# Optimization experiments

Measured on AMD Instinct MI355X. Metric: run time of the kernel, lower is better.

The kernel has to match this reference:

```python
import jax, jax.numpy as jnp
import numpy as np

EPS = 1e-5

def bn(x, p, axis):
    # p: (4,C) = [gamma, beta, running_mean, running_var]; eval-mode batchnorm
    g, b, m, v = p
    shp = [1] * x.ndim
    shp[axis] = -1
    g = g.reshape(shp); b = b.reshape(shp); m = m.reshape(shp); v = v.reshape(shp)
    return (x - m) * g * jax.lax.rsqrt(v + EPS) + b

def knn_idx(query, ref, k):
    # query (B,S,D), ref (B,N,D) -> (B,S,k) nearest-neighbor indices
    d = (jnp.sum(query * query, -1)[:, :, None]
         - 2.0 * jnp.einsum('bsd,bnd->bsn', query, ref)
         + jnp.sum(ref * ref, -1)[:, None, :])
    return jax.lax.top_k(-d, k)[1]

def fps(xyz, npoint):
    # farthest point sampling, deterministic start at index 0. xyz (B,N,3) -> (B,npoint)
    B, N, _ = xyz.shape
    def body(i, state):
        idxs, dists, far = state
        idxs = idxs.at[:, i].set(far)
        centroid = jnp.take_along_axis(xyz, far[:, None, None], axis=1)  # (B,1,3)
        d = jnp.sum((xyz - centroid) ** 2, -1)                           # (B,N)
        dists = jnp.minimum(dists, d)
        return idxs, dists, jnp.argmax(dists, -1).astype(jnp.int32)
    idxs = jnp.zeros((B, npoint), jnp.int32)
    dists = jnp.full((B, N), 1e10, xyz.dtype)
    far = jnp.zeros((B,), jnp.int32)
    idxs, _, _ = jax.lax.fori_loop(0, npoint, body, (idxs, dists, far))
    return idxs

def sample_and_group(npoint, nsample, xyz, feature):
    # xyz (B,N,3); feature (B,C,N) channel-first -> new_xyz (B,S,3), new_feature (B,S,k,2C)
    B = xyz.shape[0]
    xyz_sg = jax.lax.stop_gradient(xyz)
    fps_idx = fps(xyz_sg, npoint)                       # (B,S)
    bi = jnp.arange(B)[:, None]
    new_xyz = xyz[bi, fps_idx]                          # (B,S,3)
    ft = jnp.swapaxes(feature, 1, 2)                    # (B,N,C)
    new_pts = ft[bi, fps_idx]                           # (B,S,C)
    idx = knn_idx(jax.lax.stop_gradient(new_xyz), xyz_sg, nsample)  # (B,S,k)
    grouped = ft[jnp.arange(B)[:, None, None], idx]     # (B,S,k,C)
    centered = grouped - new_pts[:, :, None, :]
    new_feature = jnp.concatenate(
        [centered, jnp.broadcast_to(new_pts[:, :, None, :], grouped.shape)], -1)
    return new_xyz, new_feature

def local_op(x, w, bnp):
    # x (B,S,k,D); conv1d k=1 over D, bn, relu, max over neighbors -> (B,out,S)
    h = jax.nn.relu(bn(jnp.einsum('bskd,od->bsko', x, w), bnp, -1))
    return jnp.swapaxes(jnp.max(h, axis=2), 1, 2)

def edge_branch(f_t, idx, w, bnp):
    # DGCNN-style EdgeConv: concat(f_j - f_i, f_i), conv2d k=1, bn, leakyrelu, max over k
    B = f_t.shape[0]
    nb = f_t[jnp.arange(B)[:, None, None], idx]         # (B,N,k,C)
    center = jnp.broadcast_to(f_t[:, :, None, :], nb.shape)
    e = jnp.concatenate([nb - center, center], -1)      # (B,N,k,2C)
    h = jax.nn.leaky_relu(bn(jnp.einsum('bnkc,oc->bnko', e, w), bnp, -1), 0.2)
    return jnp.max(h, axis=2)                           # (B,N,C)

def dual_graph_fusion(xyz_cf, f, k, geo_w, geo_bn, feat_w, feat_bn, fuse_w, fuse_bn):
    # xyz_cf (B,3,N), f (B,C,N): one kNN graph in coordinate space, one in feature space,
    # EdgeConv on each, concat, 1x1 conv fusion -> (B,C,N)
    xyz_t = jax.lax.stop_gradient(jnp.swapaxes(xyz_cf, 1, 2))  # (B,N,3)
    f_t = jnp.swapaxes(f, 1, 2)                                # (B,N,C)
    idx_g = knn_idx(xyz_t, xyz_t, k)
    f_sg = jax.lax.stop_gradient(f_t)
    idx_f = knn_idx(f_sg, f_sg, k)
    g = edge_branch(f_t, idx_g, geo_w, geo_bn)
    h = edge_branch(f_t, idx_f, feat_w, feat_bn)
    fused = jnp.concatenate([g, h], -1)                        # (B,N,2C)
    out = jax.nn.leaky_relu(bn(jnp.einsum('bnc,oc->bno', fused, fuse_w), fuse_bn, -1), 0.2)
    return jnp.swapaxes(out, 1, 2)                             # (B,C,N)

def _bn_params(key, c):
    k1, k2, k3, k4 = jax.random.split(key, 4)
    g = jax.random.uniform(k1, (c,), minval=0.5, maxval=1.5)
    b = jax.random.normal(k2, (c,)) * 0.1
    m = jax.random.normal(k3, (c,)) * 0.1
    v = jax.random.uniform(k4, (c,), minval=0.5, maxval=1.5)
    return jnp.stack([g, b, m, v])

def setup_inputs() -> dict:
    key = jax.random.key(0)
    ks = jax.random.split(key, 20)
    B, N = 16, 2048
    def w(k, o, i):
        return jax.random.normal(k, (o, i), dtype=jnp.float32) * (1.0 / np.sqrt(i))
    return {
        'x': jax.random.normal(ks[0], (B, 6, N), dtype=jnp.float32),
        'w1': w(ks[1], 64, 6),        'bn1': _bn_params(ks[2], 64),
        'w2': w(ks[3], 1024, 64),     'bn2': _bn_params(ks[4], 1024),
        'geo_w': w(ks[5], 64, 128),   'geo_bn': _bn_params(ks[6], 64),
        'feat_w': w(ks[7], 64, 128),  'feat_bn': _bn_params(ks[8], 64),
        'fuse_w': w(ks[9], 64, 128),  'fuse_bn': _bn_params(ks[10], 64),
        'gl0_w': w(ks[11], 128, 128), 'gl0_bn': _bn_params(ks[12], 128),
        'gl1_w': w(ks[13], 256, 256), 'gl1_bn': _bn_params(ks[14], 256),
        'wf': w(ks[15], 512, 1280),   'bnf': _bn_params(ks[16], 512),
    }

def reference(x, w1, bn1, w2, bn2, geo_w, geo_bn, feat_w, feat_bn, fuse_w, fuse_bn,
              gl0_w, gl0_bn, gl1_w, gl1_bn, wf, bnf):
    B, _, N = x.shape
    xyz = jnp.swapaxes(x[:, 0:3, :], 1, 2)                                   # (B,N,3)
    f_o = jax.nn.relu(bn(jnp.einsum('bcn,oc->bon', x, w1), bn1, 1))          # (B,64,N)
    out_feat = dual_graph_fusion(x[:, 0:3, :], f_o, 20,
                                 geo_w, geo_bn, feat_w, feat_bn, fuse_w, fuse_bn)
    stride = N // 256
    x_skip = jax.nn.relu(bn(jnp.einsum('bcn,oc->bon', f_o[:, :, ::stride], w2), bn2, 1))  # (B,1024,256)
    new_xyz, nf = sample_and_group(512, 32, xyz, out_feat)
    f0 = local_op(nf, gl0_w, gl0_bn)                                         # (B,128,512)
    new_xyz, nf = sample_and_group(256, 32, new_xyz, f0)
    f1 = local_op(nf, gl1_w, gl1_bn)                                         # (B,256,256)
    f1 = jnp.concatenate([f1, x_skip], 1)                                    # (B,1280,256)
    res = jax.nn.leaky_relu(bn(jnp.einsum('bcn,oc->bon', f1, wf), bnf, 1), 0.2)  # (B,512,256)
    return res
```

## Files before the change

kernel.cpp:

```cpp
#include <hip/hip_runtime.h>
#include <float.h>
#include <math.h>


static constexpr int B_   = 16;
static constexpr int N_   = 2048;
static constexpr int NP1  = 512;
static constexpr int NP2  = 256;
static constexpr int KG   = 20;
static constexpr int NSAMP= 32;
static constexpr int CHQ  = 256;

static constexpr long OFF_FT   = 0;
static constexpr long OFF_SQ   = OFF_FT   + (long)B_*N_*64;
static constexpr long OFF_BIG  = OFF_SQ   + (long)B_*N_;
static constexpr long OFF_IDXG = OFF_BIG  + (long)B_*N_*256;
static constexpr long OFF_IDXF = OFF_IDXG + (long)B_*N_*KG;
static constexpr long OFF_OUTF = OFF_IDXF + (long)B_*N_*KG;
static constexpr long OFF_FPS1 = OFF_OUTF + (long)B_*N_*64;
static constexpr long OFF_NX1  = OFF_FPS1 + (long)B_*NP1;
static constexpr long OFF_IDX1 = OFF_NX1  + (long)B_*NP1*3;
static constexpr long OFF_F0T  = OFF_IDX1 + (long)B_*NP1*NSAMP;
static constexpr long OFF_FPS2 = OFF_F0T  + (long)B_*NP1*128;
static constexpr long OFF_NX2  = OFF_FPS2 + (long)B_*NP2;
static constexpr long OFF_IDX2 = OFF_NX2  + (long)B_*NP2*3;
static constexpr long OFF_Q1   = OFF_IDX2 + (long)B_*NP2*NSAMP;
static constexpr long OFF_V    = OFF_Q1   + (long)B_*NP1*512;
static constexpr long OFF_WPP  = OFF_V    + (long)B_*NP2*1280;
static constexpr long OFF_WPQ0 = OFF_WPP  + 256*64;
static constexpr long OFF_WPQ1 = OFF_WPQ0 + 256*64;
static constexpr long OFF_WFT  = OFF_WPQ1 + 512*128;
static constexpr long OFF_SC   = OFF_WFT  + 128*64;
static constexpr long OFF_DL1  = OFF_SC   + 4352;
static constexpr long OFF_DL2  = OFF_DL1  + (long)B_*256*8;
static constexpr long OFF_ST   = OFF_DL2  + (long)B_*512;

static constexpr int SC_S1=0, SC_T1=64, SC_SGEO=128, SC_TGEO=192, SC_SFEAT=256, SC_TFEAT=320,
   SC_SFUSE=384, SC_TFUSE=448, SC_SGL0=512, SC_TGL0=640, SC_SGL1=768, SC_TGL1=1024,
   SC_S2=1280, SC_T2=2304, SC_SF=3328, SC_TF=3840;

__device__ __forceinline__ float lrelu_(float x) { return x >= 0.0f ? x : 0.2f * x; }

template<int CTRL, int RM>
__device__ __forceinline__ float dpp_maxm(float v) {
    int o = __builtin_amdgcn_update_dpp(__float_as_int(v), __float_as_int(v),
                                        CTRL, RM, 0xF, false);
    return fmaxf(v, __int_as_float(o));
}
__device__ __forceinline__ float wave_max64_sgpr(float v) {
    v = dpp_maxm<0xB1, 0xF>(v);
    v = dpp_maxm<0x4E, 0xF>(v);
    v = dpp_maxm<0x141,0xF>(v);
    v = dpp_maxm<0x140,0xF>(v);
    v = dpp_maxm<0x142,0xA>(v);
    v = dpp_maxm<0x143,0xC>(v);
    return __int_as_float(__builtin_amdgcn_readlane(__float_as_int(v), 63));
}

template<int CTRL>
__device__ __forceinline__ unsigned dpp_minu(unsigned x) {
    unsigned o = (unsigned)__builtin_amdgcn_update_dpp(0, (int)x, CTRL, 0xF, 0xF, true);
    return o < x ? o : x;
}
__device__ __forceinline__ unsigned wave_minu(unsigned x) {
    x = dpp_minu<0xB1>(x);
    x = dpp_minu<0x4E>(x);
    x = dpp_minu<0x141>(x);
    x = dpp_minu<0x140>(x);
    { unsigned o = (unsigned)__shfl_xor((int)x, 16); x = o < x ? o : x; }
    { unsigned o = (unsigned)__shfl_xor((int)x, 32); x = o < x ? o : x; }
    return x;
}

__device__ __forceinline__ unsigned sortable_(float f) {
    unsigned u = __float_as_uint(f);
    return u ^ ((unsigned)((int)u >> 31) | 0x80000000u);
}

__global__ void k_prep(const float* __restrict__ bn1, const float* __restrict__ bn2,
                       const float* __restrict__ geow, const float* __restrict__ geobn,
                       const float* __restrict__ featw, const float* __restrict__ featbn,
                       const float* __restrict__ fusew, const float* __restrict__ fusebn,
                       const float* __restrict__ gl0w, const float* __restrict__ gl0bn,
                       const float* __restrict__ gl1w, const float* __restrict__ gl1bn,
                       const float* __restrict__ bnfp, float* __restrict__ ws)
{
    const int tid = blockIdx.x * blockDim.x + threadIdx.x;
    const int nt  = gridDim.x * blockDim.x;
    float* sc = ws + OFF_SC;
    {
        const float* ps[8]  = {bn1, geobn, featbn, fusebn, gl0bn, gl1bn, bn2, bnfp};
        const int    ch[8]  = {64, 64, 64, 64, 128, 256, 1024, 512};
        const int    so[8]  = {SC_S1, SC_SGEO, SC_SFEAT, SC_SFUSE, SC_SGL0, SC_SGL1, SC_S2, SC_SF};
        const int    to[8]  = {SC_T1, SC_TGEO, SC_TFEAT, SC_TFUSE, SC_TGL0, SC_TGL1, SC_T2, SC_TF};
        for (int g = 0; g < 8; g++) {
            const float* p = ps[g]; int C = ch[g];
            for (int i = tid; i < C; i += nt) {
                float gg = p[i], bb = p[C+i], mm = p[2*C+i], vv = p[3*C+i];
                float s = gg * (1.0f / sqrtf(vv + 1e-5f));
                sc[so[g] + i] = s;
                sc[to[g] + i] = bb - mm * s;
            }
        }
    }
    for (int j = tid; j < 256*64; j += nt) {
        int o = j >> 6, c = j & 63; float v;
        if      (o < 64)  v = geow[o*128 + c];
        else if (o < 128) v = geow[(o-64)*128 + 64 + c];
        else if (o < 192) v = featw[(o-128)*128 + c];
        else              v = featw[(o-192)*128 + 64 + c];
        ws[OFF_WPP + j] = v;
    }
    for (int j = tid; j < 256*64; j += nt) {
        int o = j >> 6, c = j & 63; float v;
        if (o < 128) v = gl0w[o*128 + c];
        else         v = gl0w[(o-128)*128 + 64 + c] - gl0w[(o-128)*128 + c];
        ws[OFF_WPQ0 + j] = v;
    }
    for (int j = tid; j < 512*128; j += nt) {
        int o = j >> 7, c = j & 127; float v;
        if (o < 256) v = gl1w[o*256 + c];
        else         v = gl1w[(o-256)*256 + 128 + c] - gl1w[(o-256)*256 + c];
        ws[OFF_WPQ1 + j] = v;
    }
    for (int j = tid; j < 128*64; j += nt) {
        int c = j >> 6, o = j & 63;
        ws[OFF_WFT + j] = fusew[o*128 + c];
    }
}

__global__ void __launch_bounds__(256) k_feat0(const float* __restrict__ x,
                                               const float* __restrict__ w1,
                                               const float* __restrict__ sc,
                                               float* __restrict__ ft, float* __restrict__ sq)
{
    const int t = threadIdx.x, lane = t & 63, w = t >> 6;
    const int pid = blockIdx.x*4 + w;
    const int b = pid >> 11, n = pid & (N_-1);
    const float* xb = x + (long)b*6*N_ + n;
    float acc = 0.0f;
    #pragma unroll
    for (int c = 0; c < 6; c++) acc += w1[lane*6 + c] * xb[(long)c*N_];
    float val = fmaxf(sc[SC_S1 + lane]*acc + sc[SC_T1 + lane], 0.0f);
    ft[((long)b*N_ + n)*64 + lane] = val;
    float v2 = val*val;
    #pragma unroll
    for (int s = 1; s < 64; s <<= 1) v2 += __shfl_xor(v2, s);
    if (lane == 0) sq[b*N_ + n] = v2;
}

template<int RPL, int KSEL>
__device__ __forceinline__ void topk_sel3(float (&v)[RPL], int lane, int* __restrict__ out)
{
    unsigned key[RPL];
    #pragma unroll
    for (int j = 0; j < RPL; j++) key[j] = sortable_(v[j]);

    unsigned consumed = 0;
    unsigned m1 = key[0]; int s1 = 0;
    unsigned m2 = 0xFFFFFFFFu; int s2 = 0;
    #pragma unroll
    for (int j = 1; j < RPL; j++) {
        unsigned kk = key[j];
        bool lt1 = kk < m1;
        bool lt2 = kk < m2;
        unsigned nm2 = lt1 ? m1 : (lt2 ? kk : m2);
        int      ns2 = lt1 ? s1 : (lt2 ? j  : s2);
        m1 = lt1 ? kk : m1;
        s1 = lt1 ? j  : s1;
        m2 = nm2; s2 = ns2;
    }
    #pragma unroll 1
    for (int k = 0; k < KSEL; k++) {
        unsigned g = wave_minu(m1);
        unsigned long long cand = __ballot(m1 == g);
        int gi;
        if (__popcll(cand) > 1) {
            int ci = (m1 == g) ? (s1*64 + lane) : 0x7FFFFFFF;
            #pragma unroll
            for (int s = 1; s < 64; s <<= 1) { int o = __shfl_xor(ci, s); ci = o < ci ? o : ci; }
            gi = ci;
        } else {
            int wl = __ffsll((long long)cand) - 1;
            gi = __builtin_amdgcn_readlane(s1, wl) * 64 + wl;
        }
        if (lane == 0) out[k] = gi;
        if (k + 1 < KSEL) {
            bool win = (m1 == g) && (s1*64 + lane == gi);
            if (win) {
                consumed |= 1u << s1;
                m1 = m2; s1 = s2;
                m2 = 0xFFFFFFFFu;
            }
            bool need = win && (m1 == 0xFFFFFFFFu);
            if (__any(need)) {
                if (need) {
                    m1 = 0xFFFFFFFFu; s1 = 0; m2 = 0xFFFFFFFFu; s2 = 0;
                    #pragma unroll
                    for (int j = 0; j < RPL; j++) {
                        unsigned kk = ((consumed >> j) & 1u) ? 0xFFFFFFFFu : key[j];
                        bool lt1 = kk < m1;
                        bool lt2 = kk < m2;
                        unsigned nm2 = lt1 ? m1 : (lt2 ? kk : m2);
                        int      ns2 = lt1 ? s1 : (lt2 ? j  : s2);
                        m1 = lt1 ? kk : m1;
                        s1 = lt1 ? j  : s1;
                        m2 = nm2; s2 = ns2;
                    }
                }
            }
        }
    }
}

template<int NREF, int RPL, int KSEL>
__device__ __forceinline__ void knn_gbody(
    const float* qp, long qBatch, int qsN, int qsD, int NQ,
    const float* rp, long rBatch, long rsN, long rsD,
    int* out, int bid)
{
    const int t = threadIdx.x, lane = t & 63, w = t >> 6;
    const int bpb = NQ / 4;
    const int b = bid / bpb;
    const int qi = (bid % bpb)*4 + w;
    const float* rb = rp + (long)b*rBatch;
    const float* qb = qp + (long)b*qBatch + (long)qi*qsN;
    float qx = qb[0], qy = qb[qsD], qz = qb[2*qsD];
    float sumq = __fadd_rn(__fadd_rn(__fmul_rn(qx,qx), __fmul_rn(qy,qy)), __fmul_rn(qz,qz));
    float v[RPL];
    #pragma unroll
    for (int j = 0; j < RPL; j++) {
        long n = j*64 + lane;
        float rx = rb[n*rsN];
        float ry = rb[n*rsN + rsD];
        float rz = rb[n*rsN + 2*rsD];
        float dot  = __fadd_rn(__fadd_rn(__fmul_rn(qx,rx), __fmul_rn(qy,ry)), __fmul_rn(qz,rz));
        float sumr = __fadd_rn(__fadd_rn(__fmul_rn(rx,rx), __fmul_rn(ry,ry)), __fmul_rn(rz,rz));
        v[j] = __fadd_rn(__fsub_rn(sumq, __fmul_rn(2.0f, dot)), sumr);
    }
    topk_sel3<RPL, KSEL>(v, lane, out + ((long)b*NQ + qi)*KSEL);
}

__device__ __forceinline__ void fps1_seg_body(
    const float* __restrict__ x, int b, int i0, int cnt,
    int* __restrict__ fps1, float* __restrict__ nx1,
    float* __restrict__ dl1s, float* __restrict__ st, float* __restrict__ smem)
{
    __builtin_amdgcn_s_setprio(3);
    const int t = threadIdx.x, lane = t & 63, wave = t >> 6;
    const float* pb = x + (long)b*6*N_;

    float4* mrgc   = (float4*)smem;
    int*    mrgi   = (int*)(smem + 32);
    int*    sidxsg = (int*)(smem + 40);
    float*  mxsg   = smem + 296;
    float*  mysg   = smem + 552;
    float*  mzsg   = smem + 808;

    float px[8], py[8], pz[8], dl[8];
    {
        const float4* a4  = (const float4*)(pb + 8*t);
        const float4* b4  = (const float4*)(pb + N_ + 8*t);
        const float4* c4p = (const float4*)(pb + 2*N_ + 8*t);
        float4 a0 = a4[0], a1 = a4[1];
        float4 b0 = b4[0], b1 = b4[1];
        float4 c0 = c4p[0], c1 = c4p[1];
        px[0]=a0.x; px[1]=a0.y; px[2]=a0.z; px[3]=a0.w;
        px[4]=a1.x; px[5]=a1.y; px[6]=a1.z; px[7]=a1.w;
        py[0]=b0.x; py[1]=b0.y; py[2]=b0.z; py[3]=b0.w;
        py[4]=b1.x; py[5]=b1.y; py[6]=b1.z; py[7]=b1.w;
        pz[0]=c0.x; pz[1]=c0.y; pz[2]=c0.z; pz[3]=c0.w;
        pz[4]=c1.x; pz[5]=c1.y; pz[6]=c1.z; pz[7]=c1.w;
    }
    int far; float cx, cy, cz;
    if (i0 == 0) {
        #pragma unroll
        for (int p = 0; p < 8; p++) dl[p] = 1e10f;
        far = 0; cx = pb[0]; cy = pb[N_]; cz = pb[2*N_];
    } else {
        const float4* ds = (const float4*)(dl1s + ((long)b*256 + t)*8);
        float4 d0 = ds[0], d1 = ds[1];
        dl[0]=d0.x; dl[1]=d0.y; dl[2]=d0.z; dl[3]=d0.w;
        dl[4]=d1.x; dl[5]=d1.y; dl[6]=d1.z; dl[7]=d1.w;
        far = __float_as_int(st[b*16+0]);
        cx = st[b*16+1]; cy = st[b*16+2]; cz = st[b*16+3];
    }

    for (int k = 0; k < cnt; k++) {
        if (t == 0) { sidxsg[k] = far; mxsg[k] = cx; mysg[k] = cy; mzsg[k] = cz; }
        float bv = -1.0f; int bp = 0;
        #pragma unroll
        for (int p = 0; p < 8; p++) {
            float dx = __fsub_rn(px[p], cx);
            float dy = __fsub_rn(py[p], cy);
            float dz = __fsub_rn(pz[p], cz);
            float d  = __fadd_rn(__fadd_rn(__fmul_rn(dx,dx), __fmul_rn(dy,dy)), __fmul_rn(dz,dz));
            float nd = fminf(dl[p], d);
            dl[p] = nd;
            if (nd > bv) { bv = nd; bp = p; }
        }
        float wx = px[0], wy = py[0], wz = pz[0];
        #pragma unroll
        for (int p = 1; p < 8; p++) {
            bool c = (bp == p);
            wx = c ? px[p] : wx; wy = c ? py[p] : wy; wz = c ? pz[p] : wz;
        }
        float gm = wave_max64_sgpr(bv);
        unsigned long long cand = __ballot(bv == gm);
        int wl = __ffsll((long long)cand) - 1;
        int   wbp = __builtin_amdgcn_readlane(bp, wl);
        float sxw = __int_as_float(__builtin_amdgcn_readlane(__float_as_int(wx), wl));
        float syw = __int_as_float(__builtin_amdgcn_readlane(__float_as_int(wy), wl));
        float szw = __int_as_float(__builtin_amdgcn_readlane(__float_as_int(wz), wl));
        int par = k & 1;
        if (lane == 0) {
            mrgc[par*4 + wave] = make_float4(sxw, syw, szw, gm);
            mrgi[par*4 + wave] = (((wave << 6) | wl) << 3) + wbp;
        }
        __syncthreads();
        float4 e0 = mrgc[par*4 + 0];
        float fv = e0.w; int fi = mrgi[par*4 + 0];
        float ncx = e0.x, ncy = e0.y, ncz = e0.z;
        #pragma unroll
        for (int w2 = 1; w2 < 4; w2++) {
            float4 e2 = mrgc[par*4 + w2]; int i2 = mrgi[par*4 + w2];
            if (e2.w > fv) { fv = e2.w; fi = i2; ncx = e2.x; ncy = e2.y; ncz = e2.z; }
        }
        far = fi; cx = ncx; cy = ncy; cz = ncz;
    }
    __syncthreads();

    int*   f1o = fps1 + b*NP1;
    float* n1o = nx1 + (long)b*NP1*3;
    for (int s = t; s < cnt; s += 256) {
        f1o[i0+s] = sidxsg[s];
        n1o[(long)(i0+s)*3+0] = mxsg[s];
        n1o[(long)(i0+s)*3+1] = mysg[s];
        n1o[(long)(i0+s)*3+2] = mzsg[s];
    }
    float4* ds = (float4*)(dl1s + ((long)b*256 + t)*8);
    ds[0] = make_float4(dl[0], dl[1], dl[2], dl[3]);
    ds[1] = make_float4(dl[4], dl[5], dl[6], dl[7]);
    if (t == 0) {
        st[b*16+0] = __int_as_float(far);
        st[b*16+1] = cx; st[b*16+2] = cy; st[b*16+3] = cz;
    }
    __builtin_amdgcn_s_setprio(0);
}

__device__ __forceinline__ void fps2_seg_body(
    int b, int i0, int cnt,
    const float* __restrict__ nx1, int* __restrict__ fps2, float* __restrict__ nx2,
    float* __restrict__ dl2s, float* __restrict__ st, float* __restrict__ smem)
{
    __builtin_amdgcn_s_setprio(3);
    const int t = threadIdx.x, lane = t & 63, wave = t >> 6;
    float4* mrgc   = (float4*)smem;
    int*    mrgi   = (int*)(smem + 32);
    int*    sidxsg = (int*)(smem + 40);
    float*  mx2    = smem + 168;
    float*  my2    = smem + 680;
    float*  mz2    = smem + 1192;

    const float* n1 = nx1 + (long)b*NP1*3;
    for (int s = t; s < NP1; s += 256) {
        mx2[s] = n1[(long)s*3+0];
        my2[s] = n1[(long)s*3+1];
        mz2[s] = n1[(long)s*3+2];
    }
    __syncthreads();

    const int n0 = t << 1;
    float ax = mx2[n0],   ay = my2[n0],   az = mz2[n0];
    float bx = mx2[n0+1], by = my2[n0+1], bz = mz2[n0+1];
    float dl0, dl1; int far2; float c2x, c2y, c2z;
    if (i0 == 0) {
        dl0 = dl1 = 1e10f; far2 = 0;
        c2x = mx2[0]; c2y = my2[0]; c2z = mz2[0];
    } else {
        dl0 = dl2s[(long)b*512 + n0];
        dl1 = dl2s[(long)b*512 + n0 + 1];
        far2 = __float_as_int(st[b*16+4]);
        c2x = st[b*16+5]; c2y = st[b*16+6]; c2z = st[b*16+7];
    }

    for (int k = 0; k < cnt; k++) {
        if (t == 0) sidxsg[k] = far2;
        float dx = __fsub_rn(ax, c2x), dy = __fsub_rn(ay, c2y), dz = __fsub_rn(az, c2z);
        float d0 = __fadd_rn(__fadd_rn(__fmul_rn(dx,dx), __fmul_rn(dy,dy)), __fmul_rn(dz,dz));
        dx = __fsub_rn(bx, c2x); dy = __fsub_rn(by, c2y); dz = __fsub_rn(bz, c2z);
        float d1 = __fadd_rn(__fadd_rn(__fmul_rn(dx,dx), __fmul_rn(dy,dy)), __fmul_rn(dz,dz));
        dl0 = fminf(dl0, d0);
        dl1 = fminf(dl1, d1);
        float bv = dl0; int bp = 0;
        if (dl1 > bv) { bv = dl1; bp = 1; }
        float wx = bp ? bx : ax, wy = bp ? by : ay, wz = bp ? bz : az;
        float gm = wave_max64_sgpr(bv);
        unsigned long long cand = __ballot(bv == gm);
        int wl = __ffsll((long long)cand) - 1;
        int   wbp = __builtin_amdgcn_readlane(bp, wl);
        float sxw = __int_as_float(__builtin_amdgcn_readlane(__float_as_int(wx), wl));
        float syw = __int_as_float(__builtin_amdgcn_readlane(__float_as_int(wy), wl));
        float szw = __int_as_float(__builtin_amdgcn_readlane(__float_as_int(wz), wl));
        int par = k & 1;
        if (lane == 0) {
            mrgc[par*4 + wave] = make_float4(sxw, syw, szw, gm);
            mrgi[par*4 + wave] = (((wave << 6) | wl) << 1) + wbp;
        }
        __syncthreads();
        float4 e0 = mrgc[par*4 + 0];
        float fv = e0.w; int fi = mrgi[par*4 + 0];
        float ncx = e0.x, ncy = e0.y, ncz = e0.z;
        #pragma unroll
        for (int w2 = 1; w2 < 4; w2++) {
            float4 e2 = mrgc[par*4 + w2]; int i2 = mrgi[par*4 + w2];
            if (e2.w > fv) { fv = e2.w; fi = i2; ncx = e2.x; ncy = e2.y; ncz = e2.z; }
        }
        far2 = fi; c2x = ncx; c2y = ncy; c2z = ncz;
    }
    __syncthreads();

    int*   f2o = fps2 + b*NP2;
    float* n2o = nx2 + (long)b*NP2*3;
    for (int s = t; s < cnt; s += 256) {
        int j = sidxsg[s];
        f2o[i0+s] = j;
        n2o[(long)(i0+s)*3+0] = mx2[j];
        n2o[(long)(i0+s)*3+1] = my2[j];
        n2o[(long)(i0+s)*3+2] = mz2[j];
    }
    dl2s[(long)b*512 + n0]     = dl0;
    dl2s[(long)b*512 + n0 + 1] = dl1;
    if (t == 0) {
        st[b*16+4] = __int_as_float(far2);
        st[b*16+5] = c2x; st[b*16+6] = c2y; st[b*16+7] = c2z;
    }
    __builtin_amdgcn_s_setprio(0);
}

__device__ __forceinline__ void dist_gemm_body(
    const float* __restrict__ ft, const float* __restrict__ sq,
    float* __restrict__ Dnew, int qbNew, int gi, float* __restrict__ smem)
{
    float* As = smem;
    float* Bs = smem + 64*68;
    const int ib = gi & 3;
    const int jb = (gi >> 2) & 31;
    const int b  = gi >> 7;
    const int t  = threadIdx.x;
    const int tx = t & 15, ty = t >> 4;
    const float* Ab = ft + ((long)b*N_ + qbNew + (long)ib*64)*64;
    const float* Bb = ft + ((long)b*N_ + (long)jb*64)*64;
    const float* sqb = sq + (long)b*N_;
    #pragma unroll
    for (int m = 0; m < 4; m++) {
        int li = t + m*256; int r = li >> 4; int c4 = li & 15;
        float4 av = *(const float4*)(Ab + (long)r*64 + c4*4);
        As[(c4*4+0)*68+r]=av.x; As[(c4*4+1)*68+r]=av.y; As[(c4*4+2)*68+r]=av.z; As[(c4*4+3)*68+r]=av.w;
        float4 bv = *(const float4*)(Bb + (long)r*64 + c4*4);
        Bs[(c4*4+0)*68+r]=bv.x; Bs[(c4*4+1)*68+r]=bv.y; Bs[(c4*4+2)*68+r]=bv.z; Bs[(c4*4+3)*68+r]=bv.w;
    }
    __syncthreads();
    float acc[4][4];
    #pragma unroll
    for (int i = 0; i < 4; i++)
        #pragma unroll
        for (int j = 0; j < 4; j++) acc[i][j] = 0.0f;
    #pragma unroll 4
    for (int k = 0; k < 64; k++) {
        float4 a  = *(const float4*)&As[k*68 + ty*4];
        float4 b4 = *(const float4*)&Bs[k*68 + tx*4];
        acc[0][0] += a.x*b4.x; acc[0][1] += a.x*b4.y; acc[0][2] += a.x*b4.z; acc[0][3] += a.x*b4.w;
        acc[1][0] += a.y*b4.x; acc[1][1] += a.y*b4.y; acc[1][2] += a.y*b4.z; acc[1][3] += a.y*b4.w;
        acc[2][0] += a.z*b4.x; acc[2][1] += a.z*b4.y; acc[2][2] += a.z*b4.z; acc[2][3] += a.z*b4.w;
        acc[3][0] += a.w*b4.x; acc[3][1] += a.w*b4.y; acc[3][2] += a.w*b4.z; acc[3][3] += a.w*b4.w;
    }
    const int i0 = ib*64 + ty*4;
    const int j0 = jb*64 + tx*4;
    #pragma unroll
    for (int ii = 0; ii < 4; ii++) {
        float sqq = sqb[qbNew + i0 + ii];
        #pragma unroll
        for (int jj = 0; jj < 4; jj++) {
            int r = j0 + jj;
            Dnew[((long)b*CHQ + i0 + ii)*N_ + r] = (sqq - 2.0f*acc[ii][jj]) + sqb[r];
        }
    }
}

__device__ __forceinline__ void proj64_body(
    int gi, int nIB, int nJB,
    const float* __restrict__ A, long aBatch, int aRow,
    const float* __restrict__ Bw,
    float* __restrict__ C, long cBatch, int cRow, int cCol0,
    int act, const float* __restrict__ sv, const float* __restrict__ tv,
    float* __restrict__ smem)
{
    float* As = smem;
    float* Bs = smem + 64*68;
    const int ib = gi % nIB;
    const int jb = (gi / nIB) % nJB;
    const int b  = gi / (nIB*nJB);
    const int t  = threadIdx.x;
    const int tx = t & 15, ty = t >> 4;
    const float* Ab = A + (long)b*aBatch + (long)(ib*64)*aRow;
    #pragma unroll
    for (int m = 0; m < 4; m++) {
        int li = t + m*256; int r = li >> 4; int c4 = li & 15;
        float4 av = *(const float4*)(Ab + (long)r*aRow + c4*4);
        As[(c4*4+0)*68+r]=av.x; As[(c4*4+1)*68+r]=av.y; As[(c4*4+2)*68+r]=av.z; As[(c4*4+3)*68+r]=av.w;
        float4 bv = *(const float4*)(Bw + (long)(jb*64 + r)*64 + c4*4);
        Bs[(c4*4+0)*68+r]=bv.x; Bs[(c4*4+1)*68+r]=bv.y; Bs[(c4*4+2)*68+r]=bv.z; Bs[(c4*4+3)*68+r]=bv.w;
    }
    __syncthreads();
    float acc[4][4];
    #pragma unroll
    for (int i = 0; i < 4; i++)
        #pragma unroll
        for (int j = 0; j < 4; j++) acc[i][j] = 0.0f;
    #pragma unroll 4
    for (int k = 0; k < 64; k++) {
        float4 a  = *(const float4*)&As[k*68 + ty*4];
        float4 b4 = *(const float4*)&Bs[k*68 + tx*4];
        acc[0][0] += a.x*b4.x; acc[0][1] += a.x*b4.y; acc[0][2] += a.x*b4.z; acc[0][3] += a.x*b4.w;
        acc[1][0] += a.y*b4.x; acc[1][1] += a.y*b4.y; acc[1][2] += a.y*b4.z; acc[1][3] += a.y*b4.w;
        acc[2][0] += a.z*b4.x; acc[2][1] += a.z*b4.y; acc[2][2] += a.z*b4.z; acc[2][3] += a.z*b4.w;
        acc[3][0] += a.w*b4.x; acc[3][1] += a.w*b4.y; acc[3][2] += a.w*b4.z; acc[3][3] += a.w*b4.w;
    }
    const int i0 = ib*64 + ty*4;
    const int j0 = jb*64 + tx*4;
    #pragma unroll
    for (int ii = 0; ii < 4; ii++)
        #pragma unroll
        for (int jj = 0; jj < 4; jj++) {
            int j = j0 + jj;
            float vv = acc[ii][jj];
            if (act == 1) vv = fmaxf(sv[j]*vv + tv[j], 0.0f);
            C[(long)b*cBatch + (long)(i0+ii)*cRow + cCol0 + j] = vv;
        }
}

__device__ __forceinline__ void sel_body(
    const float* __restrict__ Dold, int qbOld, int* __restrict__ idxf, int bid)
{
    const int t = threadIdx.x, lane = t & 63, w = t >> 6;
    const int r = bid*4 + w;
    const int b = r >> 8, qi = r & (CHQ-1);
    const float* row = Dold + ((long)b*CHQ + qi) * N_;
    float v[32];
    #pragma unroll
    for (int j = 0; j < 32; j++) v[j] = row[j*64 + lane];
    topk_sel3<32, KG>(v, lane, idxf + ((long)b*N_ + qbOld + qi)*KG);
}

__device__ __forceinline__ void edgefuse_body(
    const float* __restrict__ P, const int* __restrict__ idxg, const int* __restrict__ idxf,
    const float* __restrict__ wft, const float* __restrict__ sc,
    float* __restrict__ outf, int bid, float* __restrict__ smem)
{
    float* wt = smem;
    float* fused = smem + 8192;
    const int t = threadIdx.x, lane = t & 63, w = t >> 6;
    for (int i = t; i < 128*64; i += 256) wt[i] = wft[i];
    const int pid = bid*4 + w;
    const int b = pid >> 11, n = pid & (N_-1);
    const float* Prow = P + ((long)b*N_ + n)*256;
    const int* ig  = idxg + ((long)b*N_ + n)*KG;
    const int* ifx = idxf + ((long)b*N_ + n)*KG;
    float gmax = -FLT_MAX, hmax = -FLT_MAX;
    for (int k = 0; k < KG; k++) {
        int idg = ig[k];
        gmax = fmaxf(gmax, P[((long)b*N_ + idg)*256 + lane]);
        int idf = ifx[k];
        hmax = fmaxf(hmax, P[((long)b*N_ + idf)*256 + 128 + lane]);
    }
    float glin = gmax - Prow[lane]       + Prow[64 + lane];
    float hlin = hmax - Prow[128 + lane] + Prow[192 + lane];
    float gv = lrelu_(sc[SC_SGEO + lane]*glin + sc[SC_TGEO + lane]);
    float hv = lrelu_(sc[SC_SFEAT + lane]*hlin + sc[SC_TFEAT + lane]);
    fused[w*128 + lane]      = gv;
    fused[w*128 + 64 + lane] = hv;
    __syncthreads();
    float acc = 0.0f;
    #pragma unroll 8
    for (int c4 = 0; c4 < 32; c4++) {
        float4 f = *(const float4*)&fused[w*128 + c4*4];
        acc += f.x * wt[(c4*4+0)*64 + lane];
        acc += f.y * wt[(c4*4+1)*64 + lane];
        acc += f.z * wt[(c4*4+2)*64 + lane];
        acc += f.w * wt[(c4*4+3)*64 + lane];
    }
    float ov = lrelu_(sc[SC_SFUSE + lane]*acc + sc[SC_TFUSE + lane]);
    outf[((long)b*N_ + n)*64 + lane] = ov;
}

template<int QN, int ROWW, int CO, int MROWS, int SO>
__device__ __forceinline__ void gathermax_body(
    const float* __restrict__ Q, const int* __restrict__ knn, const int* __restrict__ fpsi,
    const float* __restrict__ sv, const float* __restrict__ tv,
    float* __restrict__ outp, int outRow, int bid)
{
    const int t = threadIdx.x, lane = t & 63, w = t >> 6;
    const int pid = bid*4 + w;
    const int b = pid / SO, s = pid % SO;
    const int* ix = knn + ((long)b*SO + s)*NSAMP;
    float mx[QN];
    #pragma unroll
    for (int q = 0; q < QN; q++) mx[q] = -FLT_MAX;
    for (int k = 0; k < NSAMP; k++) {
        int id = ix[k];
        const float* r = Q + ((long)b*MROWS + id)*ROWW;
        #pragma unroll
        for (int q = 0; q < QN; q++) mx[q] = fmaxf(mx[q], r[lane + 64*q]);
    }
    int crow = fpsi[b*SO + s];
    const float* cr = Q + ((long)b*MROWS + crow)*ROWW + CO;
    #pragma unroll
    for (int q = 0; q < QN; q++) {
        int o = lane + 64*q;
        float lin = mx[q] + cr[o];
        float val = fmaxf(sv[o]*lin + tv[o], 0.0f);
        outp[((long)b*SO + s)*outRow + o] = val;
    }
}

__global__ void __launch_bounds__(256, 4) k_geo0(
    const float* __restrict__ x, int* __restrict__ idxg,
    int* __restrict__ fps1, float* __restrict__ nx1,
    float* __restrict__ dl1s, float* __restrict__ st,
    const float* __restrict__ ft, const float* __restrict__ sq,
    float* __restrict__ D0)
{
    __shared__ float smem[8704];
    if (blockIdx.x < (unsigned)B_) {
        fps1_seg_body(x, blockIdx.x, 0, 256, fps1, nx1, dl1s, st, smem);
        return;
    }
    if (blockIdx.x < (unsigned)(B_ + 8192)) {
        knn_gbody<N_,32,KG>(x, (long)6*N_, 1, N_, N_,
                            x, (long)6*N_, 1, N_, idxg, blockIdx.x - B_);
        return;
    }
    dist_gemm_body(ft, sq, D0, 0, blockIdx.x - (B_ + 8192), smem);
}

__global__ void __launch_bounds__(256, 4) k_chain(
    const float* __restrict__ x, const float* __restrict__ ft, const float* __restrict__ sq,
    float* __restrict__ Dnew, int qbNew,
    const float* __restrict__ Dold, int qbOld,
    int* __restrict__ idxf,
    int* __restrict__ fps1, float* __restrict__ nx1,
    float* __restrict__ dl1s, float* __restrict__ st, int i0)
{
    __shared__ float smem[8704];
    if (blockIdx.x < 16u) {
        fps1_seg_body(x, blockIdx.x, i0, 32, fps1, nx1, dl1s, st, smem);
        return;
    }
    if (blockIdx.x < 1040u) {
        sel_body(Dold, qbOld, idxf, blockIdx.x - 16);
        return;
    }
    dist_gemm_body(ft, sq, Dnew, qbNew, blockIdx.x - 1040, smem);
}

__global__ void __launch_bounds__(256, 4) k_tail9(
    const float* __restrict__ x, const float* __restrict__ ft,
    const float* __restrict__ Dold, int qbOld, int* __restrict__ idxf,
    int* __restrict__ fps1, float* __restrict__ nx1,
    float* __restrict__ dl1s, float* __restrict__ st,
    const float* __restrict__ wpp, float* __restrict__ big)
{
    __shared__ float smem[8704];
    if (blockIdx.x < 16u) {
        fps1_seg_body(x, blockIdx.x, 480, 32, fps1, nx1, dl1s, st, smem);
        return;
    }
    if (blockIdx.x < 1040u) {
        sel_body(Dold, qbOld, idxf, blockIdx.x - 16);
        return;
    }
    proj64_body(blockIdx.x - 1040, 32, 4, ft, (long)N_*64, 64, wpp,
                big, (long)N_*256, 256, 0, 0, nullptr, nullptr, smem);
}

__global__ void __launch_bounds__(256, 4) k_tail10(
    const float* __restrict__ nx1, int* __restrict__ fps2, float* __restrict__ nx2,
    float* __restrict__ dl2s, float* __restrict__ st,
    const float* __restrict__ P, const int* __restrict__ idxg, const int* __restrict__ idxf,
    const float* __restrict__ wft, const float* __restrict__ sc, float* __restrict__ outf,
    const float* __restrict__ ft, const float* __restrict__ w2, float* __restrict__ V)
{
    __shared__ float smem[8704];
    if (blockIdx.x < 16u) {
        fps2_seg_body(blockIdx.x, 0, 128, nx1, fps2, nx2, dl2s, st, smem);
        return;
    }
    if (blockIdx.x < (unsigned)(16 + 8192)) {
        edgefuse_body(P, idxg, idxf, wft, sc, outf, blockIdx.x - 16, smem);
        return;
    }
    proj64_body(blockIdx.x - (16 + 8192), 4, 16, ft, (long)N_*64, 512, w2,
                V, (long)NP2*1280, 1280, 256, 1, sc + SC_S2, sc + SC_T2, smem);
}

__global__ void __launch_bounds__(256, 4) k_tail11(
    const float* __restrict__ nx1, int* __restrict__ fps2, float* __restrict__ nx2,
    float* __restrict__ dl2s, float* __restrict__ st,
    const float* __restrict__ x, int* __restrict__ idx1,
    const float* __restrict__ outf, const float* __restrict__ wpq0, float* __restrict__ big)
{
    __shared__ float smem[8704];
    if (blockIdx.x < 16u) {
        fps2_seg_body(blockIdx.x, 128, 128, nx1, fps2, nx2, dl2s, st, smem);
        return;
    }
    if (blockIdx.x < (unsigned)(16 + 2048)) {
        knn_gbody<2048,32,32>(nx1, (long)NP1*3, 3, 1, NP1,
                              x, (long)6*N_, (long)1, (long)N_, idx1, blockIdx.x - 16);
        return;
    }
    proj64_body(blockIdx.x - (16 + 2048), 32, 4, outf, (long)N_*64, 64, wpq0,
                big, (long)N_*256, 256, 0, 0, nullptr, nullptr, smem);
}

__global__ void __launch_bounds__(256, 4) k_gm0knn2(
    const float* __restrict__ big, const int* __restrict__ idx1, const int* __restrict__ fps1,
    const float* __restrict__ sc, float* __restrict__ f0t,
    const float* __restrict__ nx2, const float* __restrict__ nx1, int* __restrict__ idx2)
{
    if (blockIdx.x < 2048u) {
        gathermax_body<2,256,128,2048,512>(big, idx1, fps1,
            sc + SC_SGL0, sc + SC_TGL0, f0t, 128, blockIdx.x);
        return;
    }
    knn_gbody<512,8,32>(nx2, (long)NP2*3, 3, 1, NP2,
                        nx1, (long)NP1*3, (long)3, (long)1, idx2, blockIdx.x - 2048);
}

__global__ void __launch_bounds__(256) k_gemm(
    const float* __restrict__ A, long aBatch, int aRow,
    const float* __restrict__ Bw, long bBatch, int K,
    float* __restrict__ C, long cBatch, int cRow, int cCol0,
    int act, const float* __restrict__ sv, const float* __restrict__ tv,
    int epi)
{
    __shared__ float As[64][68];
    __shared__ float Bs[64][68];
    const int b  = blockIdx.z;
    const int ib = blockIdx.x * 64;
    const int jb = blockIdx.y * 64;
    const int t  = threadIdx.x;
    const int tx = t & 15, ty = t >> 4;
    const float* Ab = A + (long)b * aBatch;
    const float* Bb = Bw + (long)b * bBatch;
    float acc[4][4];
    #pragma unroll
    for (int i = 0; i < 4; i++)
        #pragma unroll
        for (int j = 0; j < 4; j++) acc[i][j] = 0.0f;

    for (int kb = 0; kb < K; kb += 64) {
        #pragma unroll
        for (int m = 0; m < 4; m++) {
            int li = t + m*256; int r = li >> 4; int c4 = li & 15;
            float4 av = *(const float4*)(Ab + (long)(ib + r)*aRow + kb + c4*4);
            As[c4*4+0][r] = av.x; As[c4*4+1][r] = av.y;
            As[c4*4+2][r] = av.z; As[c4*4+3][r] = av.w;
            float4 bv = *(const float4*)(Bb + (long)(jb + r)*K + kb + c4*4);
            Bs[c4*4+0][r] = bv.x; Bs[c4*4+1][r] = bv.y;
            Bs[c4*4+2][r] = bv.z; Bs[c4*4+3][r] = bv.w;
        }
        __syncthreads();
        #pragma unroll 4
        for (int k = 0; k < 64; k++) {
            float4 a  = *(const float4*)&As[k][ty*4];
            float4 b4 = *(const float4*)&Bs[k][tx*4];
            acc[0][0] += a.x*b4.x; acc[0][1] += a.x*b4.y; acc[0][2] += a.x*b4.z; acc[0][3] += a.x*b4.w;
            acc[1][0] += a.y*b4.x; acc[1][1] += a.y*b4.y; acc[1][2] += a.y*b4.z; acc[1][3] += a.y*b4.w;
            acc[2][0] += a.z*b4.x; acc[2][1] += a.z*b4.y; acc[2][2] += a.z*b4.z; acc[2][3] += a.z*b4.w;
            acc[3][0] += a.w*b4.x; acc[3][1] += a.w*b4.y; acc[3][2] += a.w*b4.z; acc[3][3] += a.w*b4.w;
        }
        __syncthreads();
    }

    const int i0 = ib + ty*4;
    const int j0 = jb + tx*4;
    if (epi == 2) {
        #pragma unroll
        for (int ii = 0; ii < 4; ii++)
            #pragma unroll
            for (int jj = 0; jj < 4; jj++) {
                int j = j0 + jj;
                float vv = lrelu_(sv[j]*acc[ii][jj] + tv[j]);
                C[(long)b*cBatch + (long)j*cRow + (i0+ii)] = vv;
            }
    } else {
        #pragma unroll
        for (int ii = 0; ii < 4; ii++)
            #pragma unroll
            for (int jj = 0; jj < 4; jj++) {
                int j = j0 + jj;
                float vv = acc[ii][jj];
                if (act == 1) vv = fmaxf(sv[j]*vv + tv[j], 0.0f);
                else if (act == 2) vv = lrelu_(sv[j]*vv + tv[j]);
                C[(long)b*cBatch + (long)(i0+ii)*cRow + cCol0 + j] = vv;
            }
    }
}

template<int QN, int ROWW, int CO, int MROWS, int SO>
__global__ void __launch_bounds__(256) k_gathermax(
    const float* __restrict__ Q, const int* __restrict__ knn, const int* __restrict__ fpsi,
    const float* __restrict__ sv, const float* __restrict__ tv,
    float* __restrict__ outp, int outRow)
{
    gathermax_body<QN,ROWW,CO,MROWS,SO>(Q, knn, fpsi, sv, tv, outp, outRow, blockIdx.x);
}

extern "C" void kernel_launch(void* const* d_in, const int* in_sizes, int n_in,
                              void* d_out, int out_size, void* d_ws, size_t ws_size,
                              hipStream_t stream)
{
    const float* x      = (const float*)d_in[0];
    const float* w1     = (const float*)d_in[1];
    const float* bn1    = (const float*)d_in[2];
    const float* w2     = (const float*)d_in[3];
    const float* bn2    = (const float*)d_in[4];
    const float* geow   = (const float*)d_in[5];
    const float* geobn  = (const float*)d_in[6];
    const float* featw  = (const float*)d_in[7];
    const float* featbn = (const float*)d_in[8];
    const float* fusew  = (const float*)d_in[9];
    const float* fusebn = (const float*)d_in[10];
    const float* gl0w   = (const float*)d_in[11];
    const float* gl0bn  = (const float*)d_in[12];
    const float* gl1w   = (const float*)d_in[13];
    const float* gl1bn  = (const float*)d_in[14];
    const float* wf     = (const float*)d_in[15];
    const float* bnfp   = (const float*)d_in[16];

    float* ws  = (float*)d_ws;
    float* out = (float*)d_out;

    float* FT   = ws + OFF_FT;
    float* SQ   = ws + OFF_SQ;
    float* BIG  = ws + OFF_BIG;
    int*   IDXG = (int*)(ws + OFF_IDXG);
    int*   IDXF = (int*)(ws + OFF_IDXF);
    float* OUTF = ws + OFF_OUTF;
    int*   FPS1 = (int*)(ws + OFF_FPS1);
    float* NX1  = ws + OFF_NX1;
    int*   IDX1 = (int*)(ws + OFF_IDX1);
    float* F0T  = ws + OFF_F0T;
    int*   FPS2 = (int*)(ws + OFF_FPS2);
    float* NX2  = ws + OFF_NX2;
    int*   IDX2 = (int*)(ws + OFF_IDX2);
    float* Q1B  = ws + OFF_Q1;
    float* V    = ws + OFF_V;
    float* WPP  = ws + OFF_WPP;
    float* WPQ0 = ws + OFF_WPQ0;
    float* WPQ1 = ws + OFF_WPQ1;
    float* WFT  = ws + OFF_WFT;
    float* SC   = ws + OFF_SC;
    float* DL1  = ws + OFF_DL1;
    float* DL2  = ws + OFF_DL2;
    float* ST   = ws + OFF_ST;

    hipLaunchKernelGGL(k_prep, dim3(64), dim3(256), 0, stream,
        bn1, bn2, geow, geobn, featw, featbn, fusew, fusebn, gl0w, gl0bn, gl1w, gl1bn, bnfp, ws);

    hipLaunchKernelGGL(k_feat0, dim3(B_*N_/4), dim3(256), 0, stream, x, w1, SC, FT, SQ);

    hipLaunchKernelGGL(k_geo0, dim3(B_ + 8192 + 2048), dim3(256), 0, stream,
        x, IDXG, FPS1, NX1, DL1, ST, FT, SQ, BIG);

    float* bufs[2] = { BIG, Q1B };
    for (int ci = 1; ci < 8; ci++) {
        hipLaunchKernelGGL(k_chain, dim3(16 + 1024 + 2048), dim3(256), 0, stream,
            x, FT, SQ,
            bufs[ci & 1], ci*CHQ,
            bufs[(ci - 1) & 1], (ci - 1)*CHQ,
            IDXF, FPS1, NX1, DL1, ST, 256 + 32*(ci - 1));
    }

    hipLaunchKernelGGL(k_tail9, dim3(16 + 1024 + 2048), dim3(256), 0, stream,
        x, FT, bufs[1], 7*CHQ, IDXF, FPS1, NX1, DL1, ST, WPP, BIG);

    hipLaunchKernelGGL(k_tail10, dim3(16 + 8192 + 1024), dim3(256), 0, stream,
        NX1, FPS2, NX2, DL2, ST,
        BIG, IDXG, IDXF, WFT, SC, OUTF,
        FT, w2, V);

    hipLaunchKernelGGL(k_tail11, dim3(16 + 2048 + 2048), dim3(256), 0, stream,
        NX1, FPS2, NX2, DL2, ST,
        x, IDX1,
        OUTF, WPQ0, BIG);

    hipLaunchKernelGGL(k_gm0knn2, dim3(2048 + 1024), dim3(256), 0, stream,
        BIG, IDX1, FPS1, SC, F0T, NX2, NX1, IDX2);

    hipLaunchKernelGGL(k_gemm, dim3(NP1/64, 512/64, B_), dim3(256), 0, stream,
        F0T, (long)NP1*128, 128, WPQ1, (long)0, 128,
        Q1B, (long)NP1*512, 512, 0, 0, nullptr, nullptr, 0);

    hipLaunchKernelGGL((k_gathermax<4,512,256,512,256>), dim3(B_*NP2/4), dim3(256), 0, stream,
        Q1B, IDX2, FPS2, SC + SC_SGL1, SC + SC_TGL1, V, 1280);

    hipLaunchKernelGGL(k_gemm, dim3(NP2/64, 512/64, B_), dim3(256), 0, stream,
        V, (long)NP2*1280, 1280, wf, (long)0, 1280,
        out, (long)512*256, 256, 0, 2, SC + SC_SF, SC + SC_TF, 2);

    (void)in_sizes; (void)n_in; (void)out_size; (void)ws_size;
}
```

Measured before the change: 710.7 us.

## Swizzle GEMM shared-memory tiles and precompute xyz squared norms for kNN

The padded 64x68 shared tiles in all GEMM paths become unpadded 64x64 tiles with an XOR swizzle on the column index. This is meant to avoid bank conflicts while shrinking LDS per block from 8704 to 8192 floats, which may raise occupancy. Separately, k_feat0 now computes the per-point xyz squared norms once into a new workspace buffer. The geometric and first-level kNN kernels read that buffer instead of recomputing the norms for every query-reference pair. The extra global load per reference replaces three multiplies and two adds.

```diff
diff --git a/kernel.cpp b/kernel.cpp
--- a/kernel.cpp
+++ b/kernel.cpp
@@ -34,6 +34,7 @@
 static constexpr long OFF_DL1  = OFF_SC   + 4352;
 static constexpr long OFF_DL2  = OFF_DL1  + (long)B_*256*8;
 static constexpr long OFF_ST   = OFF_DL2  + (long)B_*512;
+static constexpr long OFF_GSQ  = OFF_ST   + 256;
 
 static constexpr int SC_S1=0, SC_T1=64, SC_SGEO=128, SC_TGEO=192, SC_SFEAT=256, SC_TFEAT=320,
    SC_SFUSE=384, SC_TFUSE=448, SC_SGL0=512, SC_TGL0=640, SC_SGL1=768, SC_TGL1=1024,
@@ -132,7 +133,8 @@
 __global__ void __launch_bounds__(256) k_feat0(const float* __restrict__ x,
                                                const float* __restrict__ w1,
                                                const float* __restrict__ sc,
-                                               float* __restrict__ ft, float* __restrict__ sq)
+                                               float* __restrict__ ft, float* __restrict__ sq,
+                                               float* __restrict__ gsq)
 {
     const int t = threadIdx.x, lane = t & 63, w = t >> 6;
     const int pid = blockIdx.x*4 + w;
@@ -146,7 +148,12 @@
     float v2 = val*val;
     #pragma unroll
     for (int s = 1; s < 64; s <<= 1) v2 += __shfl_xor(v2, s);
-    if (lane == 0) sq[b*N_ + n] = v2;
+    if (lane == 0) {
+        sq[b*N_ + n] = v2;
+        float rx = xb[0], ry = xb[N_], rz = xb[2*N_];
+        gsq[b*N_ + n] = __fadd_rn(__fadd_rn(__fmul_rn(rx,rx), __fmul_rn(ry,ry)),
+                                  __fmul_rn(rz,rz));
+    }
 }
 
 template<int RPL, int KSEL>
@@ -213,10 +220,11 @@
     }
 }
 
-template<int NREF, int RPL, int KSEL>
+template<int NREF, int RPL, int KSEL, bool RSQ>
 __device__ __forceinline__ void knn_gbody(
     const float* qp, long qBatch, int qsN, int qsD, int NQ,
     const float* rp, long rBatch, long rsN, long rsD,
+    const float* rsq, long rsqBatch,
     int* out, int bid)
 {
     const int t = threadIdx.x, lane = t & 63, w = t >> 6;
@@ -234,8 +242,10 @@
         float rx = rb[n*rsN];
         float ry = rb[n*rsN + rsD];
         float rz = rb[n*rsN + 2*rsD];
-        float dot  = __fadd_rn(__fadd_rn(__fmul_rn(qx,rx), __fmul_rn(qy,ry)), __fmul_rn(qz,rz));
-        float sumr = __fadd_rn(__fadd_rn(__fmul_rn(rx,rx), __fmul_rn(ry,ry)), __fmul_rn(rz,rz));
+        float dot = __fadd_rn(__fadd_rn(__fmul_rn(qx,rx), __fmul_rn(qy,ry)), __fmul_rn(qz,rz));
+        float sumr;
+        if constexpr (RSQ) sumr = rsq[(long)b*rsqBatch + n];
+        else sumr = __fadd_rn(__fadd_rn(__fmul_rn(rx,rx), __fmul_rn(ry,ry)), __fmul_rn(rz,rz));
         v[j] = __fadd_rn(__fsub_rn(sumq, __fmul_rn(2.0f, dot)), sumr);
     }
     topk_sel3<RPL, KSEL>(v, lane, out + ((long)b*NQ + qi)*KSEL);
@@ -443,7 +453,7 @@
     float* __restrict__ Dnew, int qbNew, int gi, float* __restrict__ smem)
 {
     float* As = smem;
-    float* Bs = smem + 64*68;
+    float* Bs = smem + 4096;
     const int ib = gi & 3;
     const int jb = (gi >> 2) & 31;
     const int b  = gi >> 7;
@@ -455,10 +465,13 @@
     #pragma unroll
     for (int m = 0; m < 4; m++) {
         int li = t + m*256; int r = li >> 4; int c4 = li & 15;
+        int cs = r ^ ((c4 & 7) << 2);
         float4 av = *(const float4*)(Ab + (long)r*64 + c4*4);
-        As[(c4*4+0)*68+r]=av.x; As[(c4*4+1)*68+r]=av.y; As[(c4*4+2)*68+r]=av.z; As[(c4*4+3)*68+r]=av.w;
+        As[(c4*4+0)*64 + cs] = av.x; As[(c4*4+1)*64 + cs] = av.y;
+        As[(c4*4+2)*64 + cs] = av.z; As[(c4*4+3)*64 + cs] = av.w;
         float4 bv = *(const float4*)(Bb + (long)r*64 + c4*4);
-        Bs[(c4*4+0)*68+r]=bv.x; Bs[(c4*4+1)*68+r]=bv.y; Bs[(c4*4+2)*68+r]=bv.z; Bs[(c4*4+3)*68+r]=bv.w;
+        Bs[(c4*4+0)*64 + cs] = bv.x; Bs[(c4*4+1)*64 + cs] = bv.y;
+        Bs[(c4*4+2)*64 + cs] = bv.z; Bs[(c4*4+3)*64 + cs] = bv.w;
     }
     __syncthreads();
     float acc[4][4];
@@ -468,8 +481,9 @@
         for (int j = 0; j < 4; j++) acc[i][j] = 0.0f;
     #pragma unroll 4
     for (int k = 0; k < 64; k++) {
-        float4 a  = *(const float4*)&As[k*68 + ty*4];
-        float4 b4 = *(const float4*)&Bs[k*68 + tx*4];
+        int s4 = ((k >> 2) & 7) << 2;
+        float4 a  = *(const float4*)&As[k*64 + ((ty*4) ^ s4)];
+        float4 b4 = *(const float4*)&Bs[k*64 + ((tx*4) ^ s4)];
         acc[0][0] += a.x*b4.x; acc[0][1] += a.x*b4.y; acc[0][2] += a.x*b4.z; acc[0][3] += a.x*b4.w;
         acc[1][0] += a.y*b4.x; acc[1][1] += a.y*b4.y; acc[1][2] += a.y*b4.z; acc[1][3] += a.y*b4.w;
         acc[2][0] += a.z*b4.x; acc[2][1] += a.z*b4.y; acc[2][2] += a.z*b4.z; acc[2][3] += a.z*b4.w;
@@ -497,7 +511,7 @@
     float* __restrict__ smem)
 {
     float* As = smem;
-    float* Bs = smem + 64*68;
+    float* Bs = smem + 4096;
     const int ib = gi % nIB;
     const int jb = (gi / nIB) % nJB;
     const int b  = gi / (nIB*nJB);
@@ -507,10 +521,13 @@
     #pragma unroll
     for (int m = 0; m < 4; m++) {
         int li = t + m*256; int r = li >> 4; int c4 = li & 15;
+        int cs = r ^ ((c4 & 7) << 2);
         float4 av = *(const float4*)(Ab + (long)r*aRow + c4*4);
-        As[(c4*4+0)*68+r]=av.x; As[(c4*4+1)*68+r]=av.y; As[(c4*4+2)*68+r]=av.z; As[(c4*4+3)*68+r]=av.w;
+        As[(c4*4+0)*64 + cs] = av.x; As[(c4*4+1)*64 + cs] = av.y;
+        As[(c4*4+2)*64 + cs] = av.z; As[(c4*4+3)*64 + cs] = av.w;
         float4 bv = *(const float4*)(Bw + (long)(jb*64 + r)*64 + c4*4);
-        Bs[(c4*4+0)*68+r]=bv.x; Bs[(c4*4+1)*68+r]=bv.y; Bs[(c4*4+2)*68+r]=bv.z; Bs[(c4*4+3)*68+r]=bv.w;
+        Bs[(c4*4+0)*64 + cs] = bv.x; Bs[(c4*4+1)*64 + cs] = bv.y;
+        Bs[(c4*4+2)*64 + cs] = bv.z; Bs[(c4*4+3)*64 + cs] = bv.w;
     }
     __syncthreads();
     float acc[4][4];
@@ -520,8 +537,9 @@
         for (int j = 0; j < 4; j++) acc[i][j] = 0.0f;
     #pragma unroll 4
     for (int k = 0; k < 64; k++) {
-        float4 a  = *(const float4*)&As[k*68 + ty*4];
-        float4 b4 = *(const float4*)&Bs[k*68 + tx*4];
+        int s4 = ((k >> 2) & 7) << 2;
+        float4 a  = *(const float4*)&As[k*64 + ((ty*4) ^ s4)];
+        float4 b4 = *(const float4*)&Bs[k*64 + ((tx*4) ^ s4)];
         acc[0][0] += a.x*b4.x; acc[0][1] += a.x*b4.y; acc[0][2] += a.x*b4.z; acc[0][3] += a.x*b4.w;
         acc[1][0] += a.y*b4.x; acc[1][1] += a.y*b4.y; acc[1][2] += a.y*b4.z; acc[1][3] += a.y*b4.w;
         acc[2][0] += a.z*b4.x; acc[2][1] += a.z*b4.y; acc[2][2] += a.z*b4.z; acc[2][3] += a.z*b4.w;
@@ -629,16 +647,17 @@
     int* __restrict__ fps1, float* __restrict__ nx1,
     float* __restrict__ dl1s, float* __restrict__ st,
     const float* __restrict__ ft, const float* __restrict__ sq,
-    float* __restrict__ D0)
-{
-    __shared__ float smem[8704];
+    const float* __restrict__ gsq, float* __restrict__ D0)
+{
+    __shared__ float smem[8192];
     if (blockIdx.x < (unsigned)B_) {
         fps1_seg_body(x, blockIdx.x, 0, 256, fps1, nx1, dl1s, st, smem);
         return;
     }
     if (blockIdx.x < (unsigned)(B_ + 8192)) {
-        knn_gbody<N_,32,KG>(x, (long)6*N_, 1, N_, N_,
-                            x, (long)6*N_, 1, N_, idxg, blockIdx.x - B_);
+        knn_gbody<N_,32,KG,true>(x, (long)6*N_, 1, N_, N_,
+                                 x, (long)6*N_, 1, N_,
+                                 gsq, (long)N_, idxg, blockIdx.x - B_);
         return;
     }
     dist_gemm_body(ft, sq, D0, 0, blockIdx.x - (B_ + 8192), smem);
@@ -652,7 +671,7 @@
     int* __restrict__ fps1, float* __restrict__ nx1,
     float* __restrict__ dl1s, float* __restrict__ st, int i0)
 {
-    __shared__ float smem[8704];
+    __shared__ float smem[8192];
     if (blockIdx.x < 16u) {
         fps1_seg_body(x, blockIdx.x, i0, 32, fps1, nx1, dl1s, st, smem);
         return;
@@ -671,7 +690,7 @@
     float* __restrict__ dl1s, float* __restrict__ st,
     const float* __restrict__ wpp, float* __restrict__ big)
 {
-    __shared__ float smem[8704];
+    __shared__ float smem[8192];
     if (blockIdx.x < 16u) {
         fps1_seg_body(x, blockIdx.x, 480, 32, fps1, nx1, dl1s, st, smem);
         return;
@@ -707,17 +726,18 @@
 __global__ void __launch_bounds__(256, 4) k_tail11(
     const float* __restrict__ nx1, int* __restrict__ fps2, float* __restrict__ nx2,
     float* __restrict__ dl2s, float* __restrict__ st,
-    const float* __restrict__ x, int* __restrict__ idx1,
+    const float* __restrict__ x, const float* __restrict__ gsq, int* __restrict__ idx1,
     const float* __restrict__ outf, const float* __restrict__ wpq0, float* __restrict__ big)
 {
-    __shared__ float smem[8704];
+    __shared__ float smem[8192];
     if (blockIdx.x < 16u) {
         fps2_seg_body(blockIdx.x, 128, 128, nx1, fps2, nx2, dl2s, st, smem);
         return;
     }
     if (blockIdx.x < (unsigned)(16 + 2048)) {
-        knn_gbody<2048,32,32>(nx1, (long)NP1*3, 3, 1, NP1,
-                              x, (long)6*N_, (long)1, (long)N_, idx1, blockIdx.x - 16);
+        knn_gbody<2048,32,32,true>(nx1, (long)NP1*3, 3, 1, NP1,
+                                   x, (long)6*N_, (long)1, (long)N_,
+                                   gsq, (long)N_, idx1, blockIdx.x - 16);
         return;
     }
     proj64_body(blockIdx.x - (16 + 2048), 32, 4, outf, (long)N_*64, 64, wpq0,
@@ -734,8 +754,9 @@
             sc + SC_SGL0, sc + SC_TGL0, f0t, 128, blockIdx.x);
         return;
     }
-    knn_gbody<512,8,32>(nx2, (long)NP2*3, 3, 1, NP2,
-                        nx1, (long)NP1*3, (long)3, (long)1, idx2, blockIdx.x - 2048);
+    knn_gbody<512,8,32,false>(nx2, (long)NP2*3, 3, 1, NP2,
+                              nx1, (long)NP1*3, (long)3, (long)1,
+                              nullptr, 0, idx2, blockIdx.x - 2048);
 }
 
 __global__ void __launch_bounds__(256) k_gemm(
@@ -745,8 +766,8 @@
     int act, const float* __restrict__ sv, const float* __restrict__ tv,
     int epi)
 {
-    __shared__ float As[64][68];
-    __shared__ float Bs[64][68];
+    __shared__ float As[4096];
+    __shared__ float Bs[4096];
     const int b  = blockIdx.z;
     const int ib = blockIdx.x * 64;
     const int jb = blockIdx.y * 64;
@@ -764,18 +785,20 @@
         #pragma unroll
         for (int m = 0; m < 4; m++) {
             int li = t + m*256; int r = li >> 4; int c4 = li & 15;
+            int cs = r ^ ((c4 & 7) << 2);
             float4 av = *(const float4*)(Ab + (long)(ib + r)*aRow + kb + c4*4);
-            As[c4*4+0][r] = av.x; As[c4*4+1][r] = av.y;
-            As[c4*4+2][r] = av.z; As[c4*4+3][r] = av.w;
+            As[(c4*4+0)*64 + cs] = av.x; As[(c4*4+1)*64 + cs] = av.y;
+            As[(c4*4+2)*64 + cs] = av.z; As[(c4*4+3)*64 + cs] = av.w;
             float4 bv = *(const float4*)(Bb + (long)(jb + r)*K + kb + c4*4);
-            Bs[c4*4+0][r] = bv.x; Bs[c4*4+1][r] = bv.y;
-            Bs[c4*4+2][r] = bv.z; Bs[c4*4+3][r] = bv.w;
+            Bs[(c4*4+0)*64 + cs] = bv.x; Bs[(c4*4+1)*64 + cs] = bv.y;
+            Bs[(c4*4+2)*64 + cs] = bv.z; Bs[(c4*4+3)*64 + cs] = bv.w;
         }
         __syncthreads();
         #pragma unroll 4
         for (int k = 0; k < 64; k++) {
-            float4 a  = *(const float4*)&As[k][ty*4];
-            float4 b4 = *(const float4*)&Bs[k][tx*4];
+            int s4 = ((k >> 2) & 7) << 2;
+            float4 a  = *(const float4*)&As[k*64 + ((ty*4) ^ s4)];
+            float4 b4 = *(const float4*)&Bs[k*64 + ((tx*4) ^ s4)];
             acc[0][0] += a.x*b4.x; acc[0][1] += a.x*b4.y; acc[0][2] += a.x*b4.z; acc[0][3] += a.x*b4.w;
             acc[1][0] += a.y*b4.x; acc[1][1] += a.y*b4.y; acc[1][2] += a.y*b4.z; acc[1][3] += a.y*b4.w;
             acc[2][0] += a.z*b4.x; acc[2][1] += a.z*b4.y; acc[2][2] += a.z*b4.z; acc[2][3] += a.z*b4.w;
@@ -866,14 +889,15 @@
     float* DL1  = ws + OFF_DL1;
     float* DL2  = ws + OFF_DL2;
     float* ST   = ws + OFF_ST;
+    float* GSQ  = ws + OFF_GSQ;
 
     hipLaunchKernelGGL(k_prep, dim3(64), dim3(256), 0, stream,
         bn1, bn2, geow, geobn, featw, featbn, fusew, fusebn, gl0w, gl0bn, gl1w, gl1bn, bnfp, ws);
 
-    hipLaunchKernelGGL(k_feat0, dim3(B_*N_/4), dim3(256), 0, stream, x, w1, SC, FT, SQ);
+    hipLaunchKernelGGL(k_feat0, dim3(B_*N_/4), dim3(256), 0, stream, x, w1, SC, FT, SQ, GSQ);
 
     hipLaunchKernelGGL(k_geo0, dim3(B_ + 8192 + 2048), dim3(256), 0, stream,
-        x, IDXG, FPS1, NX1, DL1, ST, FT, SQ, BIG);
+        x, IDXG, FPS1, NX1, DL1, ST, FT, SQ, GSQ, BIG);
 
     float* bufs[2] = { BIG, Q1B };
     for (int ci = 1; ci < 8; ci++) {
@@ -894,7 +918,7 @@
 
     hipLaunchKernelGGL(k_tail11, dim3(16 + 2048 + 2048), dim3(256), 0, stream,
         NX1, FPS2, NX2, DL2, ST,
-        x, IDX1,
+        x, GSQ, IDX1,
         OUTF, WPQ0, BIG);
 
     hipLaunchKernelGGL(k_gm0knn2, dim3(2048 + 1024), dim3(256), 0, stream,
```

After: 660.5 us. 1.08x faster.
